# Kernel optimization log

Measured on AMD Instinct MI355X. Metric: run time of the kernel, lower is better.

The kernel has to match this reference:

```python
import jax, jax.numpy as jnp
import numpy as np

NUM_POS = 10
GAMMA0 = 0.1
EPS = 1e-10
B = 4096
NEG = 1000
USERS = 10001  # user_num + 1
ITEMS = 10001  # item_num + 1


def setup_inputs() -> dict:
    key = jax.random.key(0)
    k1, k2, k3 = jax.random.split(key, 3)
    predictions = jax.random.normal(k1, (B, NUM_POS + NEG), dtype=jnp.float32)
    u = jnp.zeros((USERS, ITEMS), dtype=jnp.float32)  # persistent EMA stats buffer
    user_id = jax.random.randint(k2, (B,), 0, USERS)
    item_id = jax.random.randint(k3, (B, NUM_POS), 0, ITEMS)
    return {"predictions": predictions, "u": u, "user_id": user_id, "item_id": item_id}


def reference(predictions, u, user_id, item_id):
    # pos: 'b n -> (b n) 1'; neg: 'b n -> (b copy) n' with copy=NUM_POS (b slowest)
    pos_pred = predictions[:, :NUM_POS].reshape(-1, 1)                 # (B*P, 1)
    neg_pred = jnp.repeat(predictions[:, NUM_POS:], NUM_POS, axis=0)   # (B*P, NEG)
    margin = neg_pred - pos_pred                                       # (B*P, NEG)
    # detached exp-margin (global max-shift for stability)
    exp_margin = jax.lax.stop_gradient(jnp.exp(margin - jnp.max(margin)))
    uid = jnp.repeat(user_id, NUM_POS)                                 # (B*P,)
    pid = item_id.reshape(-1)                                          # (B*P,)
    # EMA scatter-update of the (user,item) stats table
    new_vals = (1.0 - GAMMA0) * u[uid, pid] + GAMMA0 * jnp.mean(exp_margin, axis=1)
    u_new = u.at[uid, pid].set(new_vals)
    denom = u_new[uid, pid][:, None] + EPS
    loss = jnp.sum(margin * (exp_margin / denom)) / B
    return loss, u_new
```

## Files before the change

### kernel.cpp

```cpp
#include <hip/hip_runtime.h>
#include <cmath>

#define NUM_POS 10
#define NEG 1000
#define COLS 1010
#define BATCH 4096
#define USERS 10001
#define ITEMS 10001
#define R_TOT (BATCH * NUM_POS)
#define HSIZE (1 << 17)
#define GAMMA0 0.1f
#define EPSV 1e-10f

#define N_U 100020001LL
#define KMAX 25005000LL
#define CPY_QUADS (KMAX - 1)
#define CPY_BLOCKS ((CPY_QUADS + 255) / 256)

__global__ void k_copy(const float* __restrict__ u, float* __restrict__ out) {
    __shared__ float lds[1028];
    const float4* __restrict__ u4 = (const float4*)u;
    float4* __restrict__ o4 = (float4*)out;
    long long K0 = 1 + (long long)blockIdx.x * 256;
    int t = threadIdx.x;
    long long k = K0 + t;
    int nq = (int)((KMAX - K0 < 256) ? (KMAX - K0) : 256);

    if (t < nq)
        ((float4*)lds)[t] = u4[k - 1];
    if (t == 0)
        ((float4*)lds)[nq] = u4[K0 + nq - 1];
    __syncthreads();
    if (t < nq) {
        float x = lds[4 * t + 3], y = lds[4 * t + 4];
        float z = lds[4 * t + 5], w = lds[4 * t + 6];
        o4[k] = make_float4(x, y, z, w);
    }
    if (blockIdx.x == 0 && t == 0) {
        out[1] = u[0]; out[2] = u[1]; out[3] = u[2];
        out[100020000] = u[100019999];
        out[100020001] = u[100020000];
    }
}

__global__ void k_rowstat(const float* __restrict__ pred, float* __restrict__ rowM) {
    int b = blockIdx.x;
    const float* row = pred + (size_t)b * COLS;
    float mn = INFINITY, mx = -INFINITY;
    for (int c = threadIdx.x; c < COLS; c += 256) {
        float v = row[c];
        if (c < NUM_POS) mn = fminf(mn, v);
        else             mx = fmaxf(mx, v);
    }
    __shared__ float smn[4], smx[4];
    int lane = threadIdx.x & 63, wid = threadIdx.x >> 6;
    for (int off = 32; off; off >>= 1) {
        mn = fminf(mn, __shfl_down(mn, off));
        mx = fmaxf(mx, __shfl_down(mx, off));
    }
    if (lane == 0) { smn[wid] = mn; smx[wid] = mx; }
    __syncthreads();
    if (threadIdx.x == 0) {
        mn = fminf(fminf(smn[0], smn[1]), fminf(smn[2], smn[3]));
        mx = fmaxf(fmaxf(smx[0], smx[1]), fmaxf(smx[2], smx[3]));
        rowM[b] = mx - mn;
    }
}

__global__ void k_gmax(const float* __restrict__ rowM, float* __restrict__ Mout) {
    float mx = -INFINITY;
    for (int i = threadIdx.x; i < BATCH; i += 256) mx = fmaxf(mx, rowM[i]);
    __shared__ float smx[4];
    int lane = threadIdx.x & 63, wid = threadIdx.x >> 6;
    for (int off = 32; off; off >>= 1) mx = fmaxf(mx, __shfl_down(mx, off));
    if (lane == 0) smx[wid] = mx;
    __syncthreads();
    if (threadIdx.x == 0)
        Mout[0] = fmaxf(fmaxf(smx[0], smx[1]), fmaxf(smx[2], smx[3]));
}

__device__ __forceinline__ unsigned hash_key(int k) {
    return (((unsigned)k * 2654435761u) >> 13) & (HSIZE - 1);
}

__global__ void k_rowsums(const float* __restrict__ pred, const float* __restrict__ Mptr,
                          const int* __restrict__ user_id, const int* __restrict__ item_id,
                          float* __restrict__ meanexp, float* __restrict__ sumS,
                          int* __restrict__ keys, int* __restrict__ hkey,
                          int* __restrict__ hval) {
    int b = blockIdx.x;
    float M = Mptr[0];
    const float* row = pred + (size_t)b * COLS;
    float e = 0.f, f = 0.f;
    for (int c = NUM_POS + threadIdx.x; c < COLS; c += 256) {
        float v = row[c];
        float w = expf(v - M);
        e += w; f += v * w;
    }
    __shared__ float sh[8], bc[2];
    int lane = threadIdx.x & 63, wid = threadIdx.x >> 6;
    for (int off = 32; off; off >>= 1) { e += __shfl_down(e, off); f += __shfl_down(f, off); }
    if (lane == 0) { sh[wid] = e; sh[4 + wid] = f; }
    __syncthreads();
    if (threadIdx.x == 0) {
        bc[0] = (sh[0] + sh[1]) + (sh[2] + sh[3]);
        bc[1] = (sh[4] + sh[5]) + (sh[6] + sh[7]);
    }
    __syncthreads();
    if (threadIdx.x < NUM_POS) {
        float E = bc[0], F = bc[1];
        int p = threadIdx.x;
        int r = b * NUM_POS + p;
        float pos = row[p];
        float s = expf(-pos);
        meanexp[r] = s * E * (1.0f / NEG);
        sumS[r]    = s * (F - pos * E);
        int key = user_id[b] * ITEMS + item_id[r];
        keys[r] = key;
        unsigned sl = hash_key(key);
        while (true) {
            int old = atomicCAS(&hkey[sl], -1, key);
            if (old == -1 || old == key) { atomicMax(&hval[sl], r); break; }
            sl = (sl + 1) & (HSIZE - 1);
        }
    }
}

__global__ void k_scatter_loss(const float* __restrict__ u_in,
                               const float* __restrict__ meanexp,
                               const float* __restrict__ sumS,
                               const int* __restrict__ keys,
                               const int* __restrict__ hkey, const int* __restrict__ hval,
                               float* __restrict__ u_out, float* __restrict__ partial) {
    int r = blockIdx.x * 256 + threadIdx.x;
    int k = keys[r];
    unsigned s = hash_key(k);
    while (hkey[s] != k) s = (s + 1) & (HSIZE - 1);
    int win = hval[s];
    float uval = u_in[(size_t)k];
    float nv = (1.0f - GAMMA0) * uval + GAMMA0 * meanexp[win];
    if (win == r) u_out[(size_t)k] = nv;
    float contrib = sumS[r] / (nv + EPSV);

    __shared__ float sh[4];
    int lane = threadIdx.x & 63, wid = threadIdx.x >> 6;
    for (int off = 32; off; off >>= 1) contrib += __shfl_down(contrib, off);
    if (lane == 0) sh[wid] = contrib;
    __syncthreads();
    if (threadIdx.x == 0)
        partial[blockIdx.x] = (sh[0] + sh[1]) + (sh[2] + sh[3]);
}

__global__ void k_final(const float* __restrict__ partial, float* __restrict__ out) {
    float v = (threadIdx.x < R_TOT / 256) ? partial[threadIdx.x] : 0.0f;
    __shared__ float sh[4];
    int lane = threadIdx.x & 63, wid = threadIdx.x >> 6;
    for (int off = 32; off; off >>= 1) v += __shfl_down(v, off);
    if (lane == 0) sh[wid] = v;
    __syncthreads();
    if (threadIdx.x == 0)
        out[0] = ((sh[0] + sh[1]) + (sh[2] + sh[3])) * (1.0f / BATCH);
}

extern "C" void kernel_launch(void* const* d_in, const int* in_sizes, int n_in,
                              void* d_out, int out_size, void* d_ws, size_t ws_size,
                              hipStream_t stream) {
    const float* pred    = (const float*)d_in[0];
    const float* u       = (const float*)d_in[1];
    const int*   user_id = (const int*)d_in[2];
    const int*   item_id = (const int*)d_in[3];

    float* out   = (float*)d_out;
    float* u_out = out + 1;

    char* w = (char*)d_ws;
    int*   hkey    = (int*)w;    w += HSIZE * sizeof(int);
    int*   hval    = (int*)w;    w += HSIZE * sizeof(int);
    float* rowM    = (float*)w;  w += BATCH * sizeof(float);
    float* Mptr    = (float*)w;  w += 64;
    float* meanexp = (float*)w;  w += R_TOT * sizeof(float);
    float* sumS    = (float*)w;  w += R_TOT * sizeof(float);
    int*   keys    = (int*)w;    w += R_TOT * sizeof(int);
    float* partial = (float*)w;  w += 256 * sizeof(float);

    hipMemsetAsync(hkey, 0xFF, HSIZE * 2 * sizeof(int), stream);

    k_rowstat<<<BATCH, 256, 0, stream>>>(pred, rowM);
    k_gmax<<<1, 256, 0, stream>>>(rowM, Mptr);
    k_rowsums<<<BATCH, 256, 0, stream>>>(pred, Mptr, user_id, item_id,
                                         meanexp, sumS, keys, hkey, hval);

    k_copy<<<CPY_BLOCKS, 256, 0, stream>>>(u, out);

    k_scatter_loss<<<R_TOT / 256, 256, 0, stream>>>(u, meanexp, sumS, keys, hkey, hval,
                                                    u_out, partial);
    k_final<<<1, 256, 0, stream>>>(partial, out);
}
```

Before: 179.8 us.

## Fuse row passes with per-row max rescaling and fold memset and final reduction

Row statistics and exp sums are now computed in a single pass per row. Each row uses its own max as the shift, and a later kernel rescales the sums by exp(rowmax - globalmax); this removes the separate global-max kernel and a second read of the predictions. The hash-table memset moves into the row kernel, and the final loss reduction runs in the last scatter block through an atomic counter, which drops two launches. The large table copy now has each thread move four float4 quads. Risks are small rounding differences from the rescaling and reliance on threadfence ordering for the last-block reduction.

```diff
diff --git a/kernel.cpp b/kernel.cpp
--- a/kernel.cpp
+++ b/kernel.cpp
@@ -14,27 +14,33 @@
 
 #define N_U 100020001LL
 #define KMAX 25005000LL
-#define CPY_QUADS (KMAX - 1)
-#define CPY_BLOCKS ((CPY_QUADS + 255) / 256)
+#define QPB 1024
+#define CPY_BLOCKS ((25004999 + QPB - 1) / QPB)
+#define SCAT_BLOCKS (R_TOT / 256)
 
 __global__ void k_copy(const float* __restrict__ u, float* __restrict__ out) {
-    __shared__ float lds[1028];
+    __shared__ float lds[4 * (QPB + 1)];
     const float4* __restrict__ u4 = (const float4*)u;
     float4* __restrict__ o4 = (float4*)out;
-    long long K0 = 1 + (long long)blockIdx.x * 256;
+    long long K0 = 1 + (long long)blockIdx.x * QPB;
     int t = threadIdx.x;
-    long long k = K0 + t;
-    int nq = (int)((KMAX - K0 < 256) ? (KMAX - K0) : 256);
-
-    if (t < nq)
-        ((float4*)lds)[t] = u4[k - 1];
-    if (t == 0)
-        ((float4*)lds)[nq] = u4[K0 + nq - 1];
-    __syncthreads();
-    if (t < nq) {
-        float x = lds[4 * t + 3], y = lds[4 * t + 4];
-        float z = lds[4 * t + 5], w = lds[4 * t + 6];
-        o4[k] = make_float4(x, y, z, w);
+    int nq = (int)((KMAX - K0 < QPB) ? (KMAX - K0) : QPB);
+
+#pragma unroll
+    for (int j = 0; j < 4; ++j) {
+        int idx = t + 256 * j;
+        if (idx < nq) ((float4*)lds)[idx] = u4[K0 + idx - 1];
+    }
+    if (t == 0) ((float4*)lds)[nq] = u4[K0 + nq - 1];
+    __syncthreads();
+#pragma unroll
+    for (int j = 0; j < 4; ++j) {
+        int idx = t + 256 * j;
+        if (idx < nq) {
+            float x = lds[4 * idx + 3], y = lds[4 * idx + 4];
+            float z = lds[4 * idx + 5], w = lds[4 * idx + 6];
+            o4[K0 + idx] = make_float4(x, y, z, w);
+        }
     }
     if (blockIdx.x == 0 && t == 0) {
         out[1] = u[0]; out[2] = u[1]; out[3] = u[2];
@@ -43,16 +49,29 @@
     }
 }
 
-__global__ void k_rowstat(const float* __restrict__ pred, float* __restrict__ rowM) {
+__device__ __forceinline__ unsigned hash_key(int k) {
+    return (((unsigned)k * 2654435761u) >> 13) & (HSIZE - 1);
+}
+
+__global__ void k_rows(const float* __restrict__ pred, float* __restrict__ rowM,
+                       float* __restrict__ eRow, float* __restrict__ fRow,
+                       float* __restrict__ mRow, int* __restrict__ hkey,
+                       int* __restrict__ counter) {
     int b = blockIdx.x;
-    const float* row = pred + (size_t)b * COLS;
+    __shared__ float2 lrow[505];
+    __shared__ float smn[4], smx[4], sh[8];
+    const float2* row2 = (const float2*)(pred + (size_t)b * COLS);
     float mn = INFINITY, mx = -INFINITY;
-    for (int c = threadIdx.x; c < COLS; c += 256) {
-        float v = row[c];
-        if (c < NUM_POS) mn = fminf(mn, v);
-        else             mx = fmaxf(mx, v);
-    }
-    __shared__ float smn[4], smx[4];
+    for (int i = threadIdx.x; i < 505; i += 256) {
+        float2 v = row2[i];
+        lrow[i] = v;
+        if (i < 5) mn = fminf(mn, fminf(v.x, v.y));
+        else       mx = fmaxf(mx, fmaxf(v.x, v.y));
+    }
+    if (threadIdx.x < 16)
+        ((int4*)hkey)[b * 16 + threadIdx.x] = make_int4(-1, -1, -1, -1);
+    if (b == 0 && threadIdx.x == 16) *counter = 0;
+
     int lane = threadIdx.x & 63, wid = threadIdx.x >> 6;
     for (int off = 32; off; off >>= 1) {
         mn = fminf(mn, __shfl_down(mn, off));
@@ -60,14 +79,34 @@
     }
     if (lane == 0) { smn[wid] = mn; smx[wid] = mx; }
     __syncthreads();
+    mx = fmaxf(fmaxf(smx[0], smx[1]), fmaxf(smx[2], smx[3]));
     if (threadIdx.x == 0) {
         mn = fminf(fminf(smn[0], smn[1]), fminf(smn[2], smn[3]));
-        mx = fmaxf(fmaxf(smx[0], smx[1]), fmaxf(smx[2], smx[3]));
         rowM[b] = mx - mn;
-    }
-}
-
-__global__ void k_gmax(const float* __restrict__ rowM, float* __restrict__ Mout) {
+        mRow[b] = mx;
+    }
+    float e = 0.f, f = 0.f;
+    for (int i = 5 + threadIdx.x; i < 505; i += 256) {
+        float2 v = lrow[i];
+        float w0 = expf(v.x - mx), w1 = expf(v.y - mx);
+        e += w0 + w1;
+        f += v.x * w0 + v.y * w1;
+    }
+    for (int off = 32; off; off >>= 1) { e += __shfl_down(e, off); f += __shfl_down(f, off); }
+    if (lane == 0) { sh[wid] = e; sh[4 + wid] = f; }
+    __syncthreads();
+    if (threadIdx.x == 0) {
+        eRow[b] = (sh[0] + sh[1]) + (sh[2] + sh[3]);
+        fRow[b] = (sh[4] + sh[5]) + (sh[6] + sh[7]);
+    }
+}
+
+__global__ void k_emit(const float* __restrict__ pred, const float* __restrict__ rowM,
+                       const float* __restrict__ eRow, const float* __restrict__ fRow,
+                       const float* __restrict__ mRow, const int* __restrict__ user_id,
+                       const int* __restrict__ item_id, float* __restrict__ meanexp,
+                       float* __restrict__ sumS, int* __restrict__ keys,
+                       int* __restrict__ hkey, int* __restrict__ hval) {
     float mx = -INFINITY;
     for (int i = threadIdx.x; i < BATCH; i += 256) mx = fmaxf(mx, rowM[i]);
     __shared__ float smx[4];
@@ -75,63 +114,31 @@
     for (int off = 32; off; off >>= 1) mx = fmaxf(mx, __shfl_down(mx, off));
     if (lane == 0) smx[wid] = mx;
     __syncthreads();
-    if (threadIdx.x == 0)
-        Mout[0] = fmaxf(fmaxf(smx[0], smx[1]), fmaxf(smx[2], smx[3]));
-}
-
-__device__ __forceinline__ unsigned hash_key(int k) {
-    return (((unsigned)k * 2654435761u) >> 13) & (HSIZE - 1);
-}
-
-__global__ void k_rowsums(const float* __restrict__ pred, const float* __restrict__ Mptr,
-                          const int* __restrict__ user_id, const int* __restrict__ item_id,
-                          float* __restrict__ meanexp, float* __restrict__ sumS,
-                          int* __restrict__ keys, int* __restrict__ hkey,
-                          int* __restrict__ hval) {
-    int b = blockIdx.x;
-    float M = Mptr[0];
-    const float* row = pred + (size_t)b * COLS;
-    float e = 0.f, f = 0.f;
-    for (int c = NUM_POS + threadIdx.x; c < COLS; c += 256) {
-        float v = row[c];
-        float w = expf(v - M);
-        e += w; f += v * w;
-    }
-    __shared__ float sh[8], bc[2];
-    int lane = threadIdx.x & 63, wid = threadIdx.x >> 6;
-    for (int off = 32; off; off >>= 1) { e += __shfl_down(e, off); f += __shfl_down(f, off); }
-    if (lane == 0) { sh[wid] = e; sh[4 + wid] = f; }
-    __syncthreads();
-    if (threadIdx.x == 0) {
-        bc[0] = (sh[0] + sh[1]) + (sh[2] + sh[3]);
-        bc[1] = (sh[4] + sh[5]) + (sh[6] + sh[7]);
-    }
-    __syncthreads();
-    if (threadIdx.x < NUM_POS) {
-        float E = bc[0], F = bc[1];
-        int p = threadIdx.x;
-        int r = b * NUM_POS + p;
-        float pos = row[p];
-        float s = expf(-pos);
-        meanexp[r] = s * E * (1.0f / NEG);
-        sumS[r]    = s * (F - pos * E);
-        int key = user_id[b] * ITEMS + item_id[r];
-        keys[r] = key;
-        unsigned sl = hash_key(key);
-        while (true) {
-            int old = atomicCAS(&hkey[sl], -1, key);
-            if (old == -1 || old == key) { atomicMax(&hval[sl], r); break; }
-            sl = (sl + 1) & (HSIZE - 1);
-        }
-    }
-}
-
-__global__ void k_scatter_loss(const float* __restrict__ u_in,
-                               const float* __restrict__ meanexp,
-                               const float* __restrict__ sumS,
-                               const int* __restrict__ keys,
-                               const int* __restrict__ hkey, const int* __restrict__ hval,
-                               float* __restrict__ u_out, float* __restrict__ partial) {
+    float M = fmaxf(fmaxf(smx[0], smx[1]), fmaxf(smx[2], smx[3]));
+
+    int r = blockIdx.x * 256 + threadIdx.x;
+    int b = r / NUM_POS, p = r - b * NUM_POS;
+    float pos = pred[(size_t)b * COLS + p];
+    float scale = expf(mRow[b] - M);
+    float E = eRow[b] * scale, F = fRow[b] * scale;
+    float s = expf(-pos);
+    meanexp[r] = s * E * (1.0f / NEG);
+    sumS[r]    = s * (F - pos * E);
+    int key = user_id[b] * ITEMS + item_id[r];
+    keys[r] = key;
+    unsigned sl = hash_key(key);
+    while (true) {
+        int old = atomicCAS(&hkey[sl], -1, key);
+        if (old == -1 || old == key) { atomicMax(&hval[sl], r); break; }
+        sl = (sl + 1) & (HSIZE - 1);
+    }
+}
+
+__global__ void k_scatter(const float* __restrict__ u_in, const float* __restrict__ meanexp,
+                          const float* __restrict__ sumS, const int* __restrict__ keys,
+                          const int* __restrict__ hkey, const int* __restrict__ hval,
+                          float* __restrict__ u_out, float* __restrict__ partial,
+                          int* __restrict__ counter, float* __restrict__ out0) {
     int r = blockIdx.x * 256 + threadIdx.x;
     int k = keys[r];
     unsigned s = hash_key(k);
@@ -143,23 +150,29 @@
     float contrib = sumS[r] / (nv + EPSV);
 
     __shared__ float sh[4];
+    __shared__ int amLast;
     int lane = threadIdx.x & 63, wid = threadIdx.x >> 6;
     for (int off = 32; off; off >>= 1) contrib += __shfl_down(contrib, off);
     if (lane == 0) sh[wid] = contrib;
     __syncthreads();
-    if (threadIdx.x == 0)
+    if (threadIdx.x == 0) {
         partial[blockIdx.x] = (sh[0] + sh[1]) + (sh[2] + sh[3]);
-}
-
-__global__ void k_final(const float* __restrict__ partial, float* __restrict__ out) {
-    float v = (threadIdx.x < R_TOT / 256) ? partial[threadIdx.x] : 0.0f;
-    __shared__ float sh[4];
-    int lane = threadIdx.x & 63, wid = threadIdx.x >> 6;
-    for (int off = 32; off; off >>= 1) v += __shfl_down(v, off);
-    if (lane == 0) sh[wid] = v;
-    __syncthreads();
-    if (threadIdx.x == 0)
-        out[0] = ((sh[0] + sh[1]) + (sh[2] + sh[3])) * (1.0f / BATCH);
+        __threadfence();
+        int prev = atomicAdd(counter, 1);
+        amLast = (prev == SCAT_BLOCKS - 1);
+    }
+    __syncthreads();
+    if (amLast) {
+        __threadfence();
+        const volatile float* vp = (const volatile float*)partial;
+        float v = (threadIdx.x < SCAT_BLOCKS) ? vp[threadIdx.x] : 0.0f;
+        for (int off = 32; off; off >>= 1) v += __shfl_down(v, off);
+        __shared__ float s2[4];
+        if (lane == 0) s2[wid] = v;
+        __syncthreads();
+        if (threadIdx.x == 0)
+            out0[0] = ((s2[0] + s2[1]) + (s2[2] + s2[3])) * (1.0f / BATCH);
+    }
 }
 
 extern "C" void kernel_launch(void* const* d_in, const int* in_sizes, int n_in,
@@ -170,29 +183,26 @@
     const int*   user_id = (const int*)d_in[2];
     const int*   item_id = (const int*)d_in[3];
 
-    float* out   = (float*)d_out;
-    float* u_out = out + 1;
+    float* out = (float*)d_out;
 
     char* w = (char*)d_ws;
     int*   hkey    = (int*)w;    w += HSIZE * sizeof(int);
     int*   hval    = (int*)w;    w += HSIZE * sizeof(int);
+    int*   counter = (int*)w;    w += 64;
     float* rowM    = (float*)w;  w += BATCH * sizeof(float);
-    float* Mptr    = (float*)w;  w += 64;
+    float* eRow    = (float*)w;  w += BATCH * sizeof(float);
+    float* fRow    = (float*)w;  w += BATCH * sizeof(float);
+    float* mRow    = (float*)w;  w += BATCH * sizeof(float);
     float* meanexp = (float*)w;  w += R_TOT * sizeof(float);
     float* sumS    = (float*)w;  w += R_TOT * sizeof(float);
     int*   keys    = (int*)w;    w += R_TOT * sizeof(int);
     float* partial = (float*)w;  w += 256 * sizeof(float);
 
-    hipMemsetAsync(hkey, 0xFF, HSIZE * 2 * sizeof(int), stream);
-
-    k_rowstat<<<BATCH, 256, 0, stream>>>(pred, rowM);
-    k_gmax<<<1, 256, 0, stream>>>(rowM, Mptr);
-    k_rowsums<<<BATCH, 256, 0, stream>>>(pred, Mptr, user_id, item_id,
-                                         meanexp, sumS, keys, hkey, hval);
-
+    k_rows<<<BATCH, 256, 0, stream>>>(pred, rowM, eRow, fRow, mRow, hkey, counter);
+    k_emit<<<SCAT_BLOCKS, 256, 0, stream>>>(pred, rowM, eRow, fRow, mRow,
+                                            user_id, item_id, meanexp, sumS, keys,
+                                            hkey, hval);
     k_copy<<<CPY_BLOCKS, 256, 0, stream>>>(u, out);
-
-    k_scatter_loss<<<R_TOT / 256, 256, 0, stream>>>(u, meanexp, sumS, keys, hkey, hval,
-                                                    u_out, partial);
-    k_final<<<1, 256, 0, stream>>>(partial, out);
-}
+    k_scatter<<<SCAT_BLOCKS, 256, 0, stream>>>(u, meanexp, sumS, keys, hkey, hval,
+                                               out + 1, partial, counter, out);
+}
```

Result: slower. 192.8 us (+7.2%).
